# Performance work log

Measured on AMD Instinct MI355X. Metric: run time of the kernel, lower is better.

The kernel has to match this reference:

```python
import jax, jax.numpy as jnp
import numpy as np

N_QUBITS = 8
C64 = jnp.complex64

# ---- gate matrices ----

def u3(t, p, l):
    c = jnp.cos(t / 2).astype(C64)
    s = jnp.sin(t / 2).astype(C64)
    ep = jnp.exp(1j * p).astype(C64)
    el = jnp.exp(1j * l).astype(C64)
    return jnp.stack([jnp.stack([c, -el * s]),
                      jnp.stack([ep * s, ep * el * c])])

def ry(t):
    c = jnp.cos(t / 2).astype(C64)
    s = jnp.sin(t / 2).astype(C64)
    return jnp.stack([jnp.stack([c, -s]), jnp.stack([s, c])])

def rz(t):
    e = jnp.exp(-0.5j * t).astype(C64)
    z = jnp.zeros((), C64)
    return jnp.stack([jnp.stack([e, z]), jnp.stack([z, jnp.conj(e)])])

CNOT = jnp.array([[1, 0, 0, 0], [0, 1, 0, 0], [0, 0, 0, 1], [0, 0, 1, 0]], C64)
PX = jnp.array([[0, 1], [1, 0]], C64)
PY = jnp.array([[0, -1j], [1j, 0]], C64)
PZ = jnp.array([[1, 0], [0, -1]], C64)

# ---- batched state-vector gate application; psi: [B] + [2]*8, wire 0 = axis 1 (MSB) ----

def apply_1q(psi, U, w):
    psi = jnp.moveaxis(psi, w + 1, -1)
    psi = psi @ U.T
    return jnp.moveaxis(psi, -1, w + 1)

def apply_2q(psi, U4, w0, w1):
    psi = jnp.moveaxis(psi, (w0 + 1, w1 + 1), (-2, -1))
    sh = psi.shape
    psi = (psi.reshape(sh[:-2] + (4,)) @ U4.T).reshape(sh)
    return jnp.moveaxis(psi, (-2, -1), (w0 + 1, w1 + 1))

def u_su4(psi, p, w0, w1):
    psi = apply_1q(psi, u3(p[0], p[1], p[2]), w0)
    psi = apply_1q(psi, u3(p[3], p[4], p[5]), w1)
    psi = apply_2q(psi, CNOT, w0, w1)
    psi = apply_1q(psi, ry(p[6]), w0)
    psi = apply_1q(psi, rz(p[7]), w1)
    psi = apply_2q(psi, CNOT, w1, w0)
    psi = apply_1q(psi, ry(p[8]), w0)
    psi = apply_2q(psi, CNOT, w0, w1)
    psi = apply_1q(psi, u3(p[9], p[10], p[11]), w0)
    psi = apply_1q(psi, u3(p[12], p[13], p[14]), w1)
    return psi

LAYER1 = [(0, 1), (2, 3), (4, 5), (6, 7), (1, 2), (3, 4), (5, 6), (7, 0)]
LAYER2 = [(2, 4), (6, 0), (0, 2), (4, 6)]
LAYER3 = [(2, 6)]

def expval(psi, ops):
    phi = psi
    for M, w in ops:
        phi = apply_1q(phi, M, w)
    return jnp.real(jnp.sum(jnp.conj(psi) * phi, axis=tuple(range(1, N_QUBITS + 1))))

def circuit(x, weights):
    # amplitude embedding with normalization
    psi = (x / jnp.linalg.norm(x, axis=1, keepdims=True)).astype(C64)
    psi = psi.reshape((x.shape[0],) + (2,) * N_QUBITS)
    npc = 15
    layers = [LAYER1, LAYER1, LAYER2, LAYER2, LAYER3]
    for i, wires in enumerate(layers):
        p = weights[i * npc:(i + 1) * npc]
        for (w0, w1) in wires:
            psi = u_su4(psi, p, w0, w1)
    meas = [
        expval(psi, [(PX, 2)]), expval(psi, [(PY, 2)]), expval(psi, [(PZ, 2)]),
        expval(psi, [(PX, 6)]), expval(psi, [(PY, 6)]), expval(psi, [(PZ, 6)]),
        expval(psi, [(PX, 2), (PX, 6)]),
        expval(psi, [(PY, 2), (PY, 6)]),
        expval(psi, [(PZ, 2), (PZ, 6)]),
    ]
    return jnp.stack(meas, axis=1)  # [B, 9]


def setup_inputs() -> dict:
    key = jax.random.key(0)
    k1, k2 = jax.random.split(key)
    x = jax.random.normal(k1, (8192, 256), dtype=jnp.float32)
    weights = jax.random.normal(k2, (75,), dtype=jnp.float32)
    return {"x": x, "weights": weights}


def reference(x, weights):
    return circuit(x, weights)
```

## Files before the change

kernel.cpp:

```cpp
#include <hip/hip_runtime.h>

typedef float f32x2 __attribute__((ext_vector_type(2)));
typedef f32x2 c32;

__device__ __forceinline__ c32 mkc(float x, float y) { c32 r; r[0] = x; r[1] = y; return r; }

__device__ __forceinline__ c32 cmul(c32 a, c32 b) {
    c32 r;
    asm("v_pk_mul_f32 %0, %1, %2 op_sel:[0,0] op_sel_hi:[0,1]\n\t"
        "v_pk_fma_f32 %0, %1, %2, %0 op_sel:[1,1,0] op_sel_hi:[1,0,1] neg_lo:[1,0,0]"
        : "=&v"(r) : "v"(a), "v"(b));
    return r;
}
__device__ __forceinline__ c32 cmad(c32 a, c32 b, c32 acc) {
    asm("v_pk_fma_f32 %0, %1, %2, %0 op_sel:[0,0,0] op_sel_hi:[0,1,1]\n\t"
        "v_pk_fma_f32 %0, %1, %2, %0 op_sel:[1,1,0] op_sel_hi:[1,0,1] neg_lo:[1,0,0]"
        : "+v"(acc) : "v"(a), "v"(b));
    return acc;
}


__device__ __forceinline__ void mk_u3(float th, float ph, float la, c32 U[2][2]) {
    float ct = __cosf(0.5f * th), st = __sinf(0.5f * th);
    U[0][0] = mkc(ct, 0.f);
    U[0][1] = mkc(-__cosf(la) * st, -__sinf(la) * st);
    U[1][0] = mkc(__cosf(ph) * st, __sinf(ph) * st);
    U[1][1] = mkc(__cosf(ph + la) * ct, __sinf(ph + la) * ct);
}

__device__ __forceinline__ void lmul_kron(const c32 A[2][2], const c32 B[2][2], c32 m[4]) {
    c32 t[4];
#pragma unroll
    for (int r = 0; r < 4; ++r) {
        c32 acc = mkc(0.f, 0.f);
#pragma unroll
        for (int k = 0; k < 4; ++k)
            acc = cmad(cmul(A[r >> 1][k >> 1], B[r & 1][k >> 0 & 1]), m[k], acc);
        t[r] = acc;
    }
#pragma unroll
    for (int r = 0; r < 4; ++r) m[r] = t[r];
}

__device__ void build_col(const float* __restrict__ w, int t, c32* gml) {
    const int g = t >> 2, c = t & 3;
    const float* p = w + g * 15;
    const int c0 = c >> 1, c1 = c & 1;
    c32 A[2][2], B[2][2], m[4], tmp;

    mk_u3(p[0], p[1], p[2], A);
    mk_u3(p[3], p[4], p[5], B);
#pragma unroll
    for (int r = 0; r < 4; ++r) m[r] = cmul(A[r >> 1][c0], B[r & 1][c1]);
    tmp = m[2]; m[2] = m[3]; m[3] = tmp;
    {
        float cc = __cosf(0.5f * p[6]), s = __sinf(0.5f * p[6]);
        A[0][0] = mkc(cc, 0.f); A[0][1] = mkc(-s, 0.f);
        A[1][0] = mkc(s, 0.f);  A[1][1] = mkc(cc, 0.f);
        float cz = __cosf(0.5f * p[7]), sz = __sinf(0.5f * p[7]);
        B[0][0] = mkc(cz, -sz); B[0][1] = mkc(0.f, 0.f);
        B[1][0] = mkc(0.f, 0.f); B[1][1] = mkc(cz, sz);
        lmul_kron(A, B, m);
    }
    tmp = m[1]; m[1] = m[3]; m[3] = tmp;
    {
        float cc = __cosf(0.5f * p[8]), s = __sinf(0.5f * p[8]);
        A[0][0] = mkc(cc, 0.f); A[0][1] = mkc(-s, 0.f);
        A[1][0] = mkc(s, 0.f);  A[1][1] = mkc(cc, 0.f);
        B[0][0] = mkc(1.f, 0.f); B[0][1] = mkc(0.f, 0.f);
        B[1][0] = mkc(0.f, 0.f); B[1][1] = mkc(1.f, 0.f);
        lmul_kron(A, B, m);
    }
    tmp = m[2]; m[2] = m[3]; m[3] = tmp;
    mk_u3(p[9], p[10], p[11], A);
    mk_u3(p[12], p[13], p[14], B);
    lmul_kron(A, B, m);
#pragma unroll
    for (int r = 0; r < 4; ++r) gml[g * 16 + r * 4 + c] = m[r];
}


#define STRIDE 260

__device__ __forceinline__ int swz8(int i) { return i ^ (i >> 4); }
__host__ __device__ constexpr int cswz8(int i) { return i ^ (i >> 4); }

template<int P3, int P2, int P1, int P0>
struct BitMap {
    __device__ static int scatterDyn(int v) {
        return (((v >> 3) & 1) << P3) | (((v >> 2) & 1) << P2) |
               (((v >> 1) & 1) << P1) | ((v & 1) << P0);
    }
    static constexpr int scatter(int v) {
        return (((v >> 3) & 1) << P3) | (((v >> 2) & 1) << P2) |
               (((v >> 1) & 1) << P1) | ((v & 1) << P0);
    }
};

using WA = BitMap<7, 6, 5, 4>;  using LA = BitMap<3, 2, 1, 0>;
using WB = BitMap<3, 2, 1, 0>;  using LB = BitMap<7, 6, 5, 4>;
using WC = BitMap<7, 4, 3, 0>;  using LC = BitMap<6, 5, 2, 1>;
using WD = BitMap<7, 5, 3, 1>;  using LD = BitMap<6, 4, 2, 0>;

template<class WO, class LO, class WN, class LN>
__device__ __forceinline__ void transition2(c32* slA, c32* slB, int c,
                                            c32 sA[16], c32 sB[16]) {
    const int uo = swz8(LO::scatterDyn(c));
#pragma unroll
    for (int r = 0; r < 16; ++r) slA[uo ^ cswz8(WO::scatter(r))] = sA[r];
#pragma unroll
    for (int r = 0; r < 16; ++r) slB[uo ^ cswz8(WO::scatter(r))] = sB[r];
    const int un = swz8(LN::scatterDyn(c));
#pragma unroll
    for (int r = 0; r < 16; ++r) sA[r] = slA[un ^ cswz8(WN::scatter(r))];
#pragma unroll
    for (int r = 0; r < 16; ++r) sB[r] = slB[un ^ cswz8(WN::scatter(r))];
}

constexpr int freePos(int A, int B, int k) {
    int cnt = 0;
    for (int p = 0; p < 4; ++p)
        if (p != A && p != B) { if (cnt == k) return p; ++cnt; }
    return -1;
}

template<int A, int B>
__device__ __forceinline__ void gate(const c32 m[16], c32 s[16]) {
    constexpr int C0 = freePos(A, B, 0);
    constexpr int C1 = freePos(A, B, 1);
#pragma unroll
    for (int q = 0; q < 4; ++q) {
        const int base = ((q & 1) << C0) | (((q >> 1) & 1) << C1);
        const int i00 = base, i01 = base | (1 << B), i10 = base | (1 << A),
                  i11 = base | (1 << A) | (1 << B);
        c32 a0 = s[i00], a1 = s[i01], a2 = s[i10], a3 = s[i11];
        c32 r0 = cmul(m[0],  a0); r0 = cmad(m[1],  a1, r0); r0 = cmad(m[2],  a2, r0); r0 = cmad(m[3],  a3, r0);
        c32 r1 = cmul(m[4],  a0); r1 = cmad(m[5],  a1, r1); r1 = cmad(m[6],  a2, r1); r1 = cmad(m[7],  a3, r1);
        c32 r2 = cmul(m[8],  a0); r2 = cmad(m[9],  a1, r2); r2 = cmad(m[10], a2, r2); r2 = cmad(m[11], a3, r2);
        c32 r3 = cmul(m[12], a0); r3 = cmad(m[13], a1, r3); r3 = cmad(m[14], a2, r3); r3 = cmad(m[15], a3, r3);
        s[i00] = r0; s[i01] = r1; s[i10] = r2; s[i11] = r3;
    }
}

template<int A, int B>
__device__ __forceinline__ void gate2(const c32 m[16], c32 sA[16], c32 sB[16]) {
    gate<A, B>(m, sA);
    gate<A, B>(m, sB);
}

__device__ __forceinline__ void loadm(const c32* gml, int idx, c32 m[16]) {
#pragma unroll
    for (int k = 0; k < 16; ++k) m[k] = gml[idx * 16 + k];
}

__device__ __forceinline__ void epilogue(const c32 s[16], int c, int b,
                                         float* __restrict__ out) {
    float e0 = 0, e1 = 0, e2 = 0, e3 = 0, e4 = 0, e5 = 0, e6 = 0, e7 = 0, e8 = 0;
#pragma unroll
    for (int q = 0; q < 4; ++q) {
        const int f = ((q & 1) << 1) | ((q & 2) << 2);
        c32 a00 = s[f], a01 = s[f | 1], a10 = s[f | 4], a11 = s[f | 5];
        float n00 = a00[0] * a00[0] + a00[1] * a00[1];
        float n01 = a01[0] * a01[0] + a01[1] * a01[1];
        float n10 = a10[0] * a10[0] + a10[1] * a10[1];
        float n11 = a11[0] * a11[0] + a11[1] * a11[1];
        float z2r = a00[0] * a10[0] + a00[1] * a10[1] + a01[0] * a11[0] + a01[1] * a11[1];
        float z2i = a00[0] * a10[1] - a00[1] * a10[0] + a01[0] * a11[1] - a01[1] * a11[0];
        float z6r = a00[0] * a01[0] + a00[1] * a01[1] + a10[0] * a11[0] + a10[1] * a11[1];
        float z6i = a00[0] * a01[1] - a00[1] * a01[0] + a10[0] * a11[1] - a10[1] * a11[0];
        float w1r = a00[0] * a11[0] + a00[1] * a11[1];
        float w2r = a01[0] * a10[0] + a01[1] * a10[1];
        e0 += 2.f * z2r;  e1 += 2.f * z2i;  e2 += n00 + n01 - n10 - n11;
        e3 += 2.f * z6r;  e4 += 2.f * z6i;  e5 += n00 - n01 + n10 - n11;
        e6 += 2.f * (w1r + w2r);  e7 += 2.f * (w2r - w1r);
        e8 += n00 - n01 - n10 + n11;
    }
    float e[9] = {e0, e1, e2, e3, e4, e5, e6, e7, e8};
#pragma unroll
    for (int mm = 0; mm < 9; ++mm) {
        float vv = e[mm];
#pragma unroll
        for (int o = 8; o; o >>= 1) vv += __shfl_xor(vv, o, 64);
        e[mm] = vv;
    }
    if (c == 0) {
#pragma unroll
        for (int mm = 0; mm < 9; ++mm) out[b * 9 + mm] = e[mm];
    }
}

__global__ __launch_bounds__(64, 1) void sim_kernel(const float* __restrict__ x,
                                                    const float* __restrict__ w,
                                                    float* __restrict__ out) {
    __shared__ c32 TR[8 * STRIDE];
    __shared__ c32 GML[80];
    const int lane = threadIdx.x;
    const int st   = lane >> 4;
    const int c    = lane & 15;
    const int bA   = blockIdx.x * 8 + st;
    const int bB   = bA + 4;

    const float* xbA = x + (size_t)bA * 256 + c;
    const float* xbB = x + (size_t)bB * 256 + c;
    float vA[16], vB[16];
#pragma unroll
    for (int r = 0; r < 16; ++r) vA[r] = xbA[r << 4];
#pragma unroll
    for (int r = 0; r < 16; ++r) vB[r] = xbB[r << 4];

    if (lane < 20) build_col(w, lane, GML);

    float ssA = 0.f, ssB = 0.f;
#pragma unroll
    for (int r = 0; r < 16; ++r) { ssA = fmaf(vA[r], vA[r], ssA); ssB = fmaf(vB[r], vB[r], ssB); }
#pragma unroll
    for (int o = 8; o; o >>= 1) { ssA += __shfl_xor(ssA, o, 64); ssB += __shfl_xor(ssB, o, 64); }
    const float invA = 1.0f / sqrtf(ssA);
    const float invB = 1.0f / sqrtf(ssB);
    c32 sA[16], sB[16];
#pragma unroll
    for (int r = 0; r < 16; ++r) { sA[r] = mkc(vA[r] * invA, 0.f); sB[r] = mkc(vB[r] * invB, 0.f); }

    c32* slA = TR + st * STRIDE;
    c32* slB = TR + (st + 4) * STRIDE;
    c32 m[16];

#pragma unroll 1
    for (int pass = 0; pass < 2; ++pass) {
        loadm(GML, pass, m);
        gate2<3, 2>(m, sA, sB); gate2<1, 0>(m, sA, sB); gate2<2, 1>(m, sA, sB);
        transition2<WA, LA, WB, LB>(slA, slB, c, sA, sB);
        gate2<3, 2>(m, sA, sB); gate2<1, 0>(m, sA, sB); gate2<2, 1>(m, sA, sB);
        transition2<WB, LB, WC, LC>(slA, slB, c, sA, sB);
        gate2<2, 1>(m, sA, sB); gate2<0, 3>(m, sA, sB);
        if (pass == 0) transition2<WC, LC, WA, LA>(slA, slB, c, sA, sB);
        else           transition2<WC, LC, WD, LD>(slA, slB, c, sA, sB);
    }

#pragma unroll 1
    for (int pp = 0; pp < 2; ++pp) {
        loadm(GML, 2 + pp, m);
        gate2<2, 1>(m, sA, sB); gate2<0, 3>(m, sA, sB);
        gate2<3, 2>(m, sA, sB); gate2<1, 0>(m, sA, sB);
    }
    loadm(GML, 4, m);
    gate2<2, 0>(m, sA, sB);

    epilogue(sA, c, bA, out);
    epilogue(sB, c, bB, out);
}

extern "C" void kernel_launch(void* const* d_in, const int* in_sizes, int n_in,
                              void* d_out, int out_size, void* d_ws, size_t ws_size,
                              hipStream_t stream) {
    const float* x = (const float*)d_in[0];
    const float* w = (const float*)d_in[1];
    float* out = (float*)d_out;

    const int batch = in_sizes[0] / 256;
    const int nblocks = batch / 8;
    hipLaunchKernelGGL(sim_kernel, dim3(nblocks), dim3(64), 0, stream, x, w, out);
}
```

Before: 27.11 us.

## Precompute circuit unitary columns and apply via fp16 MFMA GEMM

The circuit is linear in the input state, so a first kernel simulates it on the 256 basis states and writes the full 256x256 unitary as fp16 real and imaginary planes into workspace. A second kernel normalizes x, multiplies it by the unitary with 16x16x32 f16 MFMA, and computes the nine expectations from the products, dividing by the squared norm. This replaces per-sample gate simulation with a dense matrix product on matrix cores. It adds a second launch and fp16 rounding of both the unitary and x, which may cost accuracy.

New measurement: 41.38 us. 1.53x slower.

```diff
diff --git a/kernel.cpp b/kernel.cpp
--- a/kernel.cpp
+++ b/kernel.cpp
@@ -2,6 +2,8 @@
 
 typedef float f32x2 __attribute__((ext_vector_type(2)));
 typedef f32x2 c32;
+typedef _Float16 f16x8 __attribute__((ext_vector_type(8)));
+typedef float f32x4 __attribute__((ext_vector_type(4)));
 
 __device__ __forceinline__ c32 mkc(float x, float y) { c32 r; r[0] = x; r[1] = y; return r; }
 
@@ -35,7 +37,7 @@
         c32 acc = mkc(0.f, 0.f);
 #pragma unroll
         for (int k = 0; k < 4; ++k)
-            acc = cmad(cmul(A[r >> 1][k >> 1], B[r & 1][k >> 0 & 1]), m[k], acc);
+            acc = cmad(cmul(A[r >> 1][k >> 1], B[r & 1][k & 1]), m[k], acc);
         t[r] = acc;
     }
 #pragma unroll
@@ -153,73 +155,24 @@
     for (int k = 0; k < 16; ++k) m[k] = gml[idx * 16 + k];
 }
 
-__device__ __forceinline__ void epilogue(const c32 s[16], int c, int b,
-                                         float* __restrict__ out) {
-    float e0 = 0, e1 = 0, e2 = 0, e3 = 0, e4 = 0, e5 = 0, e6 = 0, e7 = 0, e8 = 0;
-#pragma unroll
-    for (int q = 0; q < 4; ++q) {
-        const int f = ((q & 1) << 1) | ((q & 2) << 2);
-        c32 a00 = s[f], a01 = s[f | 1], a10 = s[f | 4], a11 = s[f | 5];
-        float n00 = a00[0] * a00[0] + a00[1] * a00[1];
-        float n01 = a01[0] * a01[0] + a01[1] * a01[1];
-        float n10 = a10[0] * a10[0] + a10[1] * a10[1];
-        float n11 = a11[0] * a11[0] + a11[1] * a11[1];
-        float z2r = a00[0] * a10[0] + a00[1] * a10[1] + a01[0] * a11[0] + a01[1] * a11[1];
-        float z2i = a00[0] * a10[1] - a00[1] * a10[0] + a01[0] * a11[1] - a01[1] * a11[0];
-        float z6r = a00[0] * a01[0] + a00[1] * a01[1] + a10[0] * a11[0] + a10[1] * a11[1];
-        float z6i = a00[0] * a01[1] - a00[1] * a01[0] + a10[0] * a11[1] - a10[1] * a11[0];
-        float w1r = a00[0] * a11[0] + a00[1] * a11[1];
-        float w2r = a01[0] * a10[0] + a01[1] * a10[1];
-        e0 += 2.f * z2r;  e1 += 2.f * z2i;  e2 += n00 + n01 - n10 - n11;
-        e3 += 2.f * z6r;  e4 += 2.f * z6i;  e5 += n00 - n01 + n10 - n11;
-        e6 += 2.f * (w1r + w2r);  e7 += 2.f * (w2r - w1r);
-        e8 += n00 - n01 - n10 + n11;
-    }
-    float e[9] = {e0, e1, e2, e3, e4, e5, e6, e7, e8};
-#pragma unroll
-    for (int mm = 0; mm < 9; ++mm) {
-        float vv = e[mm];
-#pragma unroll
-        for (int o = 8; o; o >>= 1) vv += __shfl_xor(vv, o, 64);
-        e[mm] = vv;
-    }
-    if (c == 0) {
-#pragma unroll
-        for (int mm = 0; mm < 9; ++mm) out[b * 9 + mm] = e[mm];
-    }
-}
-
-__global__ __launch_bounds__(64, 1) void sim_kernel(const float* __restrict__ x,
-                                                    const float* __restrict__ w,
-                                                    float* __restrict__ out) {
+__global__ __launch_bounds__(64, 1) void basis_kernel(const float* __restrict__ w,
+                                                      _Float16* __restrict__ U16) {
     __shared__ c32 TR[8 * STRIDE];
     __shared__ c32 GML[80];
     const int lane = threadIdx.x;
     const int st   = lane >> 4;
     const int c    = lane & 15;
-    const int bA   = blockIdx.x * 8 + st;
-    const int bB   = bA + 4;
-
-    const float* xbA = x + (size_t)bA * 256 + c;
-    const float* xbB = x + (size_t)bB * 256 + c;
-    float vA[16], vB[16];
-#pragma unroll
-    for (int r = 0; r < 16; ++r) vA[r] = xbA[r << 4];
-#pragma unroll
-    for (int r = 0; r < 16; ++r) vB[r] = xbB[r << 4];
+    const int jA   = blockIdx.x * 8 + st;
+    const int jB   = jA + 4;
 
     if (lane < 20) build_col(w, lane, GML);
 
-    float ssA = 0.f, ssB = 0.f;
-#pragma unroll
-    for (int r = 0; r < 16; ++r) { ssA = fmaf(vA[r], vA[r], ssA); ssB = fmaf(vB[r], vB[r], ssB); }
-#pragma unroll
-    for (int o = 8; o; o >>= 1) { ssA += __shfl_xor(ssA, o, 64); ssB += __shfl_xor(ssB, o, 64); }
-    const float invA = 1.0f / sqrtf(ssA);
-    const float invB = 1.0f / sqrtf(ssB);
     c32 sA[16], sB[16];
 #pragma unroll
-    for (int r = 0; r < 16; ++r) { sA[r] = mkc(vA[r] * invA, 0.f); sB[r] = mkc(vB[r] * invB, 0.f); }
+    for (int r = 0; r < 16; ++r) {
+        sA[r] = mkc((r == (jA >> 4) && c == (jA & 15)) ? 1.f : 0.f, 0.f);
+        sB[r] = mkc((r == (jB >> 4) && c == (jB & 15)) ? 1.f : 0.f, 0.f);
+    }
 
     c32* slA = TR + st * STRIDE;
     c32* slB = TR + (st + 4) * STRIDE;
@@ -236,7 +189,6 @@
         if (pass == 0) transition2<WC, LC, WA, LA>(slA, slB, c, sA, sB);
         else           transition2<WC, LC, WD, LD>(slA, slB, c, sA, sB);
     }
-
 #pragma unroll 1
     for (int pp = 0; pp < 2; ++pp) {
         loadm(GML, 2 + pp, m);
@@ -246,8 +198,129 @@
     loadm(GML, 4, m);
     gate2<2, 0>(m, sA, sB);
 
-    epilogue(sA, c, bA, out);
-    epilogue(sB, c, bB, out);
+#pragma unroll
+    for (int r = 0; r < 16; ++r) {
+        const int i = WD::scatter(r) | LD::scatterDyn(c);
+        U16[(size_t)i * 256 + jA]         = (_Float16)sA[r][0];
+        U16[(size_t)(i + 256) * 256 + jA] = (_Float16)sA[r][1];
+        U16[(size_t)i * 256 + jB]         = (_Float16)sB[r][0];
+        U16[(size_t)(i + 256) * 256 + jB] = (_Float16)sB[r][1];
+    }
+}
+
+
+__global__ __launch_bounds__(256) void gemm_expect_kernel(const float* __restrict__ x,
+                                                          const _Float16* __restrict__ U16,
+                                                          float* __restrict__ out) {
+    __shared__ _Float16 Bl[32][264];
+    __shared__ float nn[32];
+    __shared__ float red[4][2][16][9];
+    const int tid = threadIdx.x;
+    const int wave = tid >> 6, lane = tid & 63;
+    const int bs = blockIdx.x * 32;
+
+    {
+        const int n = tid >> 3, sub = tid & 7;
+        const float4* xr = reinterpret_cast<const float4*>(x + (size_t)(bs + n) * 256 + sub * 32);
+        float ssq = 0.f;
+#pragma unroll
+        for (int q = 0; q < 8; ++q) {
+            float4 v = xr[q];
+            ssq = fmaf(v.x, v.x, fmaf(v.y, v.y, fmaf(v.z, v.z, fmaf(v.w, v.w, ssq))));
+            const int k0 = sub * 32 + q * 4;
+            Bl[n][k0 + 0] = (_Float16)v.x;
+            Bl[n][k0 + 1] = (_Float16)v.y;
+            Bl[n][k0 + 2] = (_Float16)v.z;
+            Bl[n][k0 + 3] = (_Float16)v.w;
+        }
+#pragma unroll
+        for (int o = 4; o; o >>= 1) ssq += __shfl_xor(ssq, o, 64);
+        if (sub == 0) nn[n] = ssq;
+    }
+    __syncthreads();
+
+    f32x4 acc[2][4][2];
+#pragma unroll
+    for (int ri = 0; ri < 2; ++ri)
+#pragma unroll
+        for (int a = 0; a < 4; ++a)
+#pragma unroll
+            for (int nt = 0; nt < 2; ++nt) acc[ri][a][nt] = (f32x4){0.f, 0.f, 0.f, 0.f};
+
+    const int ml = lane & 15, g = lane >> 4;
+    const _Float16* Abase[2][4];
+#pragma unroll
+    for (int ri = 0; ri < 2; ++ri)
+#pragma unroll
+        for (int a = 0; a < 4; ++a)
+            Abase[ri][a] = U16 + (size_t)(64 * wave + 16 * a + 256 * ri + ml) * 256 + g * 8;
+
+#pragma unroll
+    for (int kt = 0; kt < 8; ++kt) {
+        f16x8 bf[2];
+#pragma unroll
+        for (int nt = 0; nt < 2; ++nt)
+            bf[nt] = *reinterpret_cast<const f16x8*>(&Bl[nt * 16 + ml][kt * 32 + g * 8]);
+#pragma unroll
+        for (int ri = 0; ri < 2; ++ri)
+#pragma unroll
+            for (int a = 0; a < 4; ++a) {
+                f16x8 af = *reinterpret_cast<const f16x8*>(Abase[ri][a] + kt * 32);
+#pragma unroll
+                for (int nt = 0; nt < 2; ++nt)
+                    acc[ri][a][nt] = __builtin_amdgcn_mfma_f32_16x16x32_f16(af, bf[nt], acc[ri][a][nt], 0, 0, 0);
+            }
+    }
+
+#pragma unroll
+    for (int nt = 0; nt < 2; ++nt) {
+        float E[9];
+#pragma unroll
+        for (int m = 0; m < 9; ++m) E[m] = 0.f;
+#pragma unroll
+        for (int a = 0; a < 4; ++a) {
+#pragma unroll
+            for (int r = 0; r < 4; ++r) {
+                float re = acc[0][a][nt][r], im = acc[1][a][nt][r];
+                float pr = re * re + im * im;
+                E[2] += (a & 2) ? -pr : pr;
+                E[5] += (r & 2) ? -pr : pr;
+                E[8] += ((a ^ r) & 2) ? -pr : pr;
+                if (a < 2) {
+                    float pre = acc[0][a + 2][nt][r], pim = acc[1][a + 2][nt][r];
+                    E[0] += 2.f * (re * pre + im * pim);
+                    E[1] += 2.f * (re * pim - im * pre);
+                    float dre = acc[0][a + 2][nt][r ^ 2], dim = acc[1][a + 2][nt][r ^ 2];
+                    float dr = re * dre + im * dim;
+                    E[6] += 2.f * dr;
+                    E[7] += (r & 2) ? 2.f * dr : -2.f * dr;
+                }
+                if (!(r & 2)) {
+                    float qre = acc[0][a][nt][r + 2], qim = acc[1][a][nt][r + 2];
+                    E[3] += 2.f * (re * qre + im * qim);
+                    E[4] += 2.f * (re * qim - im * qre);
+                }
+            }
+        }
+#pragma unroll
+        for (int m = 0; m < 9; ++m) {
+            E[m] += __shfl_xor(E[m], 16, 64);
+            E[m] += __shfl_xor(E[m], 32, 64);
+            if (lane < 16) red[wave][nt][lane][m] = E[m];
+        }
+    }
+    __syncthreads();
+
+    if (tid < 32) {
+        const int nt = tid >> 4, nc = tid & 15;
+        const float innv = 1.0f / nn[tid];
+#pragma unroll
+        for (int m = 0; m < 9; ++m) {
+            float e = red[0][nt][nc][m] + red[1][nt][nc][m] +
+                      red[2][nt][nc][m] + red[3][nt][nc][m];
+            out[(size_t)(bs + tid) * 9 + m] = e * innv;
+        }
+    }
 }
 
 extern "C" void kernel_launch(void* const* d_in, const int* in_sizes, int n_in,
@@ -256,8 +329,11 @@
     const float* x = (const float*)d_in[0];
     const float* w = (const float*)d_in[1];
     float* out = (float*)d_out;
+    _Float16* U16 = (_Float16*)d_ws;
+
+    hipLaunchKernelGGL(basis_kernel, dim3(32), dim3(64), 0, stream, w, U16);
 
     const int batch = in_sizes[0] / 256;
-    const int nblocks = batch / 8;
-    hipLaunchKernelGGL(sim_kernel, dim3(nblocks), dim3(64), 0, stream, x, w, out);
-}
+    const int nblocks = batch / 32;
+    hipLaunchKernelGGL(gemm_expect_kernel, dim3(nblocks), dim3(256), 0, stream, x, U16, out);
+}
```
